# Optimization experiments

Measured on AMD Instinct MI355X. Metric: run time of the kernel, lower is better.

Reference implementation:

```python
import jax, jax.numpy as jnp
import numpy as np

N, M, C, CSKIP, K = 16384, 4096, 256, 128, 3
BIG = 1e10  # distance penalty for cross-batch pairs


def setup_inputs() -> dict:
    key = jax.random.key(0)
    ks = jax.random.split(key, 6)
    return {
        "x": jax.random.normal(ks[0], (M, C), jnp.float32),
        "pos": jax.random.normal(ks[1], (M, 3), jnp.float32),
        "batch": jnp.zeros((M,), jnp.int32),
        "x_skip": jax.random.normal(ks[2], (N, CSKIP), jnp.float32),
        "pos_skip": jax.random.normal(ks[3], (N, 3), jnp.float32),
        "batch_skip": jnp.zeros((N,), jnp.int32),
        "W1": jax.random.normal(ks[4], (C + CSKIP, 256), jnp.float32) * (1.0 / np.sqrt(C + CSKIP)),
        "b1": jnp.zeros((256,), jnp.float32),
        "W2": jax.random.normal(ks[5], (256, 256), jnp.float32) * (1.0 / np.sqrt(256)),
        "b2": jnp.zeros((256,), jnp.float32),
    }


def _knn_idx(pos, pos_skip, batch, batch_skip, k):
    # Squared distances via GEMM form: [N, M]
    a2 = jnp.sum(pos_skip * pos_skip, axis=-1, keepdims=True)      # [N,1]
    b2 = jnp.sum(pos * pos, axis=-1)[None, :]                       # [1,M]
    d2 = a2 + b2 - 2.0 * (pos_skip @ pos.T)                         # [N,M]
    d2 = jnp.where(batch_skip[:, None] != batch[None, :], BIG, d2)
    _, idx = jax.lax.top_k(-d2, k)                                  # [N,k]
    return idx


def reference(x, pos, batch, x_skip, pos_skip, batch_skip, W1, b1, W2, b2):
    idx = _knn_idx(pos, pos_skip, batch, batch_skip, K)             # [N,k] coarse neighbor ids
    # Exact squared dist recomputed from gathered positions (matches torch diff path)
    diff = pos_skip[:, None, :] - pos[idx]                          # [N,k,3]
    d2 = jnp.sum(diff * diff, axis=-1, keepdims=True)               # [N,k,1]
    w = 1.0 / (d2 + 1e-8)                                           # inverse-distance weights
    wsum = jnp.sum(w, axis=1, keepdims=True)                        # per-row scatter_add == sum over k
    w = w / (wsum + 1e-8)
    x_interp = jnp.sum(w * x[idx], axis=1)                          # [N,C]
    h = jnp.concatenate([x_interp, x_skip], axis=1)                 # [N,C+C']
    h = jax.nn.relu(h @ W1 + b1)
    h = jax.nn.relu(h @ W2 + b2)
    return h
```

## Files before the change

### kernel.cpp

```cpp
#include <hip/hip_runtime.h>

typedef float     f4   __attribute__((ext_vector_type(4)));
typedef float     f32x4 __attribute__((ext_vector_type(4)));
typedef _Float16  h8   __attribute__((ext_vector_type(8)));
typedef _Float16  h4   __attribute__((ext_vector_type(4)));
typedef int       i4   __attribute__((ext_vector_type(4)));

#define NQ   16384
#define MP   4096
#define CF   256
#define CSK  128
#define K1   384
#define HID  256
#define QB   16

__global__ __launch_bounds__(256) void knn_kernel(
    const float* __restrict__ pos,
    const float* __restrict__ pos_skip,
    int*   __restrict__ idx_out,
    float* __restrict__ w_out)
{
    __shared__ float          px[MP];
    __shared__ float          py[MP];
    __shared__ float          pz[MP];
    __shared__ unsigned short ci[QB][96];
    __shared__ unsigned short ci2[QB][16][3];

    const int tid = threadIdx.x;

    for (int j = tid; j < MP; j += 256) {
        px[j] = pos[3*j+0];
        py[j] = pos[3*j+1];
        pz[j] = pos[3*j+2];
    }
    __syncthreads();

    const int lane = tid & 63;
    const int wv   = tid >> 6;

    float qx[4], qy[4], qz[4];
    #pragma unroll
    for (int k = 0; k < 4; k++) {
        const int q = blockIdx.x * QB + wv * 4 + k;
        qx[k] = pos_skip[3*q+0];
        qy[k] = pos_skip[3*q+1];
        qz[k] = pos_skip[3*q+2];
    }

    unsigned K0[4], K1v[4], K2[4];
    #pragma unroll
    for (int k = 0; k < 4; k++) { K0[k] = ~0u; K1v[k] = ~0u; K2[k] = ~0u; }

    #define EVAL(PX, PY, PZ, J)                                               \
        _Pragma("unroll")                                                     \
        for (int k = 0; k < 4; k++) {                                         \
            const float dx = qx[k] - (PX), dy = qy[k] - (PY),                 \
                        dz = qz[k] - (PZ);                                    \
            const float dd = fmaf(dx, dx, fmaf(dy, dy, dz * dz));             \
            const unsigned key = (__float_as_uint(dd) & 0xFFFFF000u) | (J);   \
            const unsigned h0 = max(K0[k], key);                              \
            K0[k] = min(K0[k], key);                                          \
            const unsigned n1 = min(K1v[k], h0);                              \
            const unsigned h1 = max(K1v[k], h0);                              \
            K1v[k] = n1;                                                      \
            K2[k] = min(K2[k], h1);                                           \
        }

    float c0x = px[lane],       c1x = px[lane + 64],
          c2x = px[lane + 128], c3x = px[lane + 192];
    float c0y = py[lane],       c1y = py[lane + 64],
          c2y = py[lane + 128], c3y = py[lane + 192];
    float c0z = pz[lane],       c1z = pz[lane + 64],
          c2z = pz[lane + 128], c3z = pz[lane + 192];

    for (int it = 0; it < 64; it += 4) {
        const unsigned jb = it * 64 + lane;
        const float nx0 = px[jb + 256], nx1 = px[jb + 320],
                    nx2 = px[jb + 384], nx3 = px[jb + 448];
        const float ny0 = py[jb + 256], ny1 = py[jb + 320],
                    ny2 = py[jb + 384], ny3 = py[jb + 448];
        const float nz0 = pz[jb + 256], nz1 = pz[jb + 320],
                    nz2 = pz[jb + 384], nz3 = pz[jb + 448];
        EVAL(c0x, c0y, c0z, jb);
        EVAL(c1x, c1y, c1z, jb + 64);
        EVAL(c2x, c2y, c2z, jb + 128);
        EVAL(c3x, c3y, c3z, jb + 192);
        c0x = nx0; c1x = nx1; c2x = nx2; c3x = nx3;
        c0y = ny0; c1y = ny1; c2y = ny2; c3y = ny3;
        c0z = nz0; c1z = nz1; c2z = nz2; c3z = nz3;
    }
    #undef EVAL

    #pragma unroll
    for (int k = 0; k < 4; k++) {
        const unsigned b0 = (unsigned)__builtin_amdgcn_ds_swizzle((int)K0[k],  0x041F);
        const unsigned b1 = (unsigned)__builtin_amdgcn_ds_swizzle((int)K1v[k], 0x041F);
        const unsigned b2 = (unsigned)__builtin_amdgcn_ds_swizzle((int)K2[k],  0x041F);
        const unsigned m0 = min(K0[k], b0);
        const unsigned c1 = max(K0[k], b0);
        const unsigned d0 = min(K1v[k], b1), d1 = max(K1v[k], b1);
        const unsigned m1 = min(c1, d0);
        const unsigned m2 = min(min(max(c1, d0), d1), min(K2[k], b2));
        if (!(lane & 1)) {
            const int q = wv * 4 + k;
            const int pr = lane >> 1;
            ci[q][pr*3+0] = (unsigned short)(m0 & 0xFFFu);
            ci[q][pr*3+1] = (unsigned short)(m1 & 0xFFFu);
            ci[q][pr*3+2] = (unsigned short)(m2 & 0xFFFu);
        }
    }
    __syncthreads();

    {
        const int q    = tid >> 4;
        const int part = tid & 15;
        const int g    = blockIdx.x * QB + q;
        const double qxd = (double)pos_skip[3*g+0];
        const double qyd = (double)pos_skip[3*g+1];
        const double qzd = (double)pos_skip[3*g+2];
        const double a2d = qxd*qxd + qyd*qyd + qzd*qzd;

        double e0 = 1e300, e1 = 1e300, e2 = 1e300;
        int    j0 = 0,     j1 = 0,     j2 = 0;
        #pragma unroll
        for (int c = 0; c < 6; c++) {
            const int j = ci[q][part*6 + c];
            const double pxd = (double)px[j], pyd = (double)py[j],
                         pzd = (double)pz[j];
            const double b2  = pxd*pxd + pyd*pyd + pzd*pzd;
            const double dot = qxd*pxd + qyd*pyd + qzd*pzd;
            const double d   = (a2d + b2) - 2.0 * dot;
            if (d < e2) {
                if (d < e1) {
                    e2 = e1; j2 = j1;
                    if (d < e0) { e1 = e0; j1 = j0; e0 = d; j0 = j; }
                    else        { e1 = d;  j1 = j; }
                } else { e2 = d; j2 = j; }
            }
        }
        ci2[q][part][0] = (unsigned short)j0;
        ci2[q][part][1] = (unsigned short)j1;
        ci2[q][part][2] = (unsigned short)j2;
    }
    __syncthreads();

    if (tid < QB) {
        const int g = blockIdx.x * QB + tid;
        const double qxd = (double)pos_skip[3*g+0];
        const double qyd = (double)pos_skip[3*g+1];
        const double qzd = (double)pos_skip[3*g+2];
        const double a2d = qxd*qxd + qyd*qyd + qzd*qzd;

        double e0 = 1e300, e1 = 1e300, e2 = 1e300;
        int    j0 = 0,     j1 = 0,     j2 = 0;
        for (int p = 0; p < 16; p++) {
            #pragma unroll
            for (int s = 0; s < 3; s++) {
                const int j = ci2[tid][p][s];
                const double pxd = (double)px[j], pyd = (double)py[j],
                             pzd = (double)pz[j];
                const double b2  = pxd*pxd + pyd*pyd + pzd*pzd;
                const double dot = qxd*pxd + qyd*pyd + qzd*pzd;
                const double d   = (a2d + b2) - 2.0 * dot;
                if (d < e2) {
                    if (d < e1) {
                        e2 = e1; j2 = j1;
                        if (d < e0) { e1 = e0; j1 = j0; e0 = d; j0 = j; }
                        else        { e1 = d;  j1 = j; }
                    } else { e2 = d; j2 = j; }
                }
            }
        }
        const float sx = pos_skip[3*g+0], sy = pos_skip[3*g+1], sz = pos_skip[3*g+2];
        const int jj[3] = { j0, j1, j2 };
        float wv3[3];
        #pragma unroll
        for (int k = 0; k < 3; k++) {
            const float dx = sx - px[jj[k]], dy = sy - py[jj[k]],
                        dz = sz - pz[jj[k]];
            const float dd = dx*dx + dy*dy + dz*dz;
            wv3[k] = 1.0f / (dd + 1e-8f);
        }
        const float inv = 1.0f / (wv3[0] + wv3[1] + wv3[2] + 1e-8f);
        #pragma unroll
        for (int k = 0; k < 3; k++) {
            idx_out[g*3+k] = jj[k];
            w_out[g*3+k]   = wv3[k] * inv;
        }
    }
}

__global__ __launch_bounds__(256) void wconv_kernel(
    const float* __restrict__ W1, const float* __restrict__ W2,
    _Float16* __restrict__ Wt1, _Float16* __restrict__ Wt2)
{
    const int i = blockIdx.x * 256 + threadIdx.x;
    if (i < K1 * HID) {
        const int k = i >> 8, n = i & 255;
        Wt1[(size_t)(k >> 5) * 8192 + ((k >> 3) & 3) * 2048 + n * 8 + (k & 7)]
            = (_Float16)W1[i];
    } else {
        const int i2 = i - K1 * HID;
        const int k = i2 >> 8, n = i2 & 255;
        Wt2[(size_t)(k >> 5) * 8192 + ((k >> 3) & 3) * 2048 + n * 8 + (k & 7)]
            = (_Float16)W2[i2];
    }
}

__global__ __launch_bounds__(256) void mlp_kernel(
    const float* __restrict__ x,
    const float* __restrict__ x_skip,
    const _Float16* __restrict__ Wt1,
    const _Float16* __restrict__ Wt2,
    const float* __restrict__ b1,
    const float* __restrict__ b2,
    const int*   __restrict__ nidx,
    const float* __restrict__ nw,
    float* __restrict__ out)
{
    __shared__ _Float16 As[32][392];
    _Float16 (*Hs)[264] = reinterpret_cast<_Float16 (*)[264]>(&As[0][0]);

    const int tid  = threadIdx.x;
    const int row0 = blockIdx.x * 32;

    {
        const int r   = tid >> 3;
        const int sub = tid & 7;
        const int g   = row0 + r;
        const int j0 = nidx[g*3+0], j1 = nidx[g*3+1], j2 = nidx[g*3+2];
        const float w0 = nw[g*3+0], w1 = nw[g*3+1], w2 = nw[g*3+2];
        const f4* xa = (const f4*)(x + (size_t)j0 * CF);
        const f4* xb = (const f4*)(x + (size_t)j1 * CF);
        const f4* xc = (const f4*)(x + (size_t)j2 * CF);
        const f4* xs = (const f4*)(x_skip + (size_t)g * CSK);
        #pragma unroll
        for (int t = 0; t < 8; t++) {
            const int c4 = t * 8 + sub;
            const f4 a = xa[c4], b = xb[c4], c = xc[c4];
            const f4 v = a * w0 + b * w1 + c * w2;
            h4 hv; hv[0]=(_Float16)v[0]; hv[1]=(_Float16)v[1];
                   hv[2]=(_Float16)v[2]; hv[3]=(_Float16)v[3];
            *(h4*)&As[r][c4 * 4] = hv;
        }
        #pragma unroll
        for (int t = 0; t < 4; t++) {
            const int c4 = t * 8 + sub;
            const f4 v = xs[c4];
            h4 hv; hv[0]=(_Float16)v[0]; hv[1]=(_Float16)v[1];
                   hv[2]=(_Float16)v[2]; hv[3]=(_Float16)v[3];
            *(h4*)&As[r][CF + c4 * 4] = hv;
        }
    }

    const int ln   = tid & 15;
    const int quad = (tid >> 4) & 3;
    const int wv_  = tid >> 6;
    const int nb   = wv_ * 64;
    const int q8   = quad * 8;

    const _Float16* w1b = Wt1 + quad * 2048 + (size_t)(nb + ln) * 8;
    const _Float16* w2b = Wt2 + quad * 2048 + (size_t)(nb + ln) * 8;

    f32x4 acc[2][4];
    #pragma unroll
    for (int mt = 0; mt < 2; mt++)
        #pragma unroll
        for (int nt = 0; nt < 4; nt++) acc[mt][nt] = (f32x4)0.0f;

    h8 B[3][4];
    #pragma unroll
    for (int s = 0; s < 3; s++)
        #pragma unroll
        for (int nt = 0; nt < 4; nt++)
            B[s][nt] = *(const h8*)(w1b + (size_t)s * 8192 + nt * 128);

    __syncthreads();

    #pragma unroll
    for (int kb = 0; kb < 12; kb++) {
        const int s = kb % 3;
        h8 ha[2];
        #pragma unroll
        for (int mt = 0; mt < 2; mt++)
            ha[mt] = *(const h8*)&As[mt*16 + ln][kb*32 + q8];
        h8 hb[4];
        #pragma unroll
        for (int nt = 0; nt < 4; nt++) hb[nt] = B[s][nt];
        if (kb < 9) {
            #pragma unroll
            for (int nt = 0; nt < 4; nt++)
                B[s][nt] = *(const h8*)(w1b + (size_t)(kb+3) * 8192 + nt * 128);
        } else {
            #pragma unroll
            for (int nt = 0; nt < 4; nt++)
                B[s][nt] = *(const h8*)(w2b + (size_t)(kb-9) * 8192 + nt * 128);
        }
        #pragma unroll
        for (int mt = 0; mt < 2; mt++)
            #pragma unroll
            for (int nt = 0; nt < 4; nt++)
                acc[mt][nt] = __builtin_amdgcn_mfma_f32_16x16x32_f16(
                    ha[mt], hb[nt], acc[mt][nt], 0, 0, 0);
    }
    __syncthreads();

    #pragma unroll
    for (int nt = 0; nt < 4; nt++) {
        const int n = nb + nt*16 + ln;
        const float bv = b1[n];
        #pragma unroll
        for (int mt = 0; mt < 2; mt++) {
            #pragma unroll
            for (int r = 0; r < 4; r++) {
                const int m = mt*16 + quad*4 + r;
                Hs[m][n] = (_Float16)fmaxf(acc[mt][nt][r] + bv, 0.0f);
            }
            acc[mt][nt] = (f32x4)0.0f;
        }
    }
    __syncthreads();

    #pragma unroll
    for (int kb = 0; kb < 8; kb++) {
        const int s = kb % 3;
        h8 ha[2];
        #pragma unroll
        for (int mt = 0; mt < 2; mt++)
            ha[mt] = *(const h8*)&Hs[mt*16 + ln][kb*32 + q8];
        h8 hb[4];
        #pragma unroll
        for (int nt = 0; nt < 4; nt++) hb[nt] = B[s][nt];
        if (kb < 5) {
            #pragma unroll
            for (int nt = 0; nt < 4; nt++)
                B[s][nt] = *(const h8*)(w2b + (size_t)(kb+3) * 8192 + nt * 128);
        }
        #pragma unroll
        for (int mt = 0; mt < 2; mt++)
            #pragma unroll
            for (int nt = 0; nt < 4; nt++)
                acc[mt][nt] = __builtin_amdgcn_mfma_f32_16x16x32_f16(
                    ha[mt], hb[nt], acc[mt][nt], 0, 0, 0);
    }

    #pragma unroll
    for (int nt = 0; nt < 4; nt++) {
        const int n = nb + nt*16 + ln;
        const float bv = b2[n];
        #pragma unroll
        for (int mt = 0; mt < 2; mt++)
            #pragma unroll
            for (int r = 0; r < 4; r++) {
                const int m = mt*16 + quad*4 + r;
                out[(size_t)(row0 + m) * HID + n] = fmaxf(acc[mt][nt][r] + bv, 0.0f);
            }
    }
}

extern "C" void kernel_launch(void* const* d_in, const int* in_sizes, int n_in,
                              void* d_out, int out_size, void* d_ws, size_t ws_size,
                              hipStream_t stream) {
    const float* x         = (const float*)d_in[0];
    const float* pos       = (const float*)d_in[1];
    const float* x_skip    = (const float*)d_in[3];
    const float* pos_skip  = (const float*)d_in[4];
    const float* W1        = (const float*)d_in[6];
    const float* b1        = (const float*)d_in[7];
    const float* W2        = (const float*)d_in[8];
    const float* b2        = (const float*)d_in[9];
    float* out = (float*)d_out;

    char* ws = (char*)d_ws;
    int*      nidx = (int*)ws;
    float*    nw   = (float*)(ws + 196608);
    _Float16* Wt1  = (_Float16*)(ws + 393216);
    _Float16* Wt2  = (_Float16*)(ws + 589824);

    wconv_kernel<<<(K1*HID + HID*HID) / 256, 256, 0, stream>>>(W1, W2, Wt1, Wt2);
    knn_kernel<<<NQ / QB, 256, 0, stream>>>(pos, pos_skip, nidx, nw);
    mlp_kernel<<<NQ / 32, 256, 0, stream>>>(x, x_skip, Wt1, Wt2, b1, b2, nidx, nw, out);
}
```

Before: 129.7 us.

## Fuse kNN search and MLP into one kernel with 32 queries per block

Merges the kNN kernel and the MLP kernel into a single kernel. Neighbor indices and weights now stay in shared memory instead of going through a global workspace, and the shared memory used for positions is reused for the MLP A/H tiles. Queries per block go from 16 to 32, so each wave tracks 8 queries, which spreads the 48KB position load over more work and halves the kNN grid. The costs are higher register pressure from the 8-query top-3 state, lower occupancy from about 57KB of shared memory, and no overlap between the kNN compute phase and the GEMM phase of other blocks.

```diff
diff --git a/kernel.cpp b/kernel.cpp
--- a/kernel.cpp
+++ b/kernel.cpp
@@ -12,19 +12,45 @@
 #define CSK  128
 #define K1   384
 #define HID  256
-#define QB   16
-
-__global__ __launch_bounds__(256) void knn_kernel(
+
+__global__ __launch_bounds__(256) void wconv_kernel(
+    const float* __restrict__ W1, const float* __restrict__ W2,
+    _Float16* __restrict__ Wt1, _Float16* __restrict__ Wt2)
+{
+    const int i = blockIdx.x * 256 + threadIdx.x;
+    if (i < K1 * HID) {
+        const int k = i >> 8, n = i & 255;
+        Wt1[(size_t)(k >> 5) * 8192 + ((k >> 3) & 3) * 2048 + n * 8 + (k & 7)]
+            = (_Float16)W1[i];
+    } else {
+        const int i2 = i - K1 * HID;
+        const int k = i2 >> 8, n = i2 & 255;
+        Wt2[(size_t)(k >> 5) * 8192 + ((k >> 3) & 3) * 2048 + n * 8 + (k & 7)]
+            = (_Float16)W2[i2];
+    }
+}
+
+__global__ __launch_bounds__(256) void fused_kernel(
     const float* __restrict__ pos,
     const float* __restrict__ pos_skip,
-    int*   __restrict__ idx_out,
-    float* __restrict__ w_out)
+    const float* __restrict__ x,
+    const float* __restrict__ x_skip,
+    const _Float16* __restrict__ Wt1,
+    const _Float16* __restrict__ Wt2,
+    const float* __restrict__ b1,
+    const float* __restrict__ b2,
+    float* __restrict__ out)
 {
-    __shared__ float          px[MP];
-    __shared__ float          py[MP];
-    __shared__ float          pz[MP];
-    __shared__ unsigned short ci[QB][96];
-    __shared__ unsigned short ci2[QB][16][3];
+    __shared__ __align__(16) char smem[57600];
+    float* px = (float*)smem;
+    float* py = (float*)(smem + 16384);
+    float* pz = (float*)(smem + 32768);
+    unsigned short (*ci)[96]    = (unsigned short (*)[96])(smem + 49152);
+    unsigned short (*ci2)[8][3] = (unsigned short (*)[8][3])(smem + 55296);
+    int   (*fidx)[3] = (int (*)[3])(smem + 56832);
+    float (*fw)[3]   = (float (*)[3])(smem + 57216);
+    _Float16 (*As)[392] = (_Float16 (*)[392])smem;
+    _Float16 (*Hs)[264] = (_Float16 (*)[264])smem;
 
     const int tid = threadIdx.x;
 
@@ -38,83 +64,85 @@
     const int lane = tid & 63;
     const int wv   = tid >> 6;
 
-    float qx[4], qy[4], qz[4];
-    #pragma unroll
-    for (int k = 0; k < 4; k++) {
-        const int q = blockIdx.x * QB + wv * 4 + k;
-        qx[k] = pos_skip[3*q+0];
-        qy[k] = pos_skip[3*q+1];
-        qz[k] = pos_skip[3*q+2];
-    }
-
-    unsigned K0[4], K1v[4], K2[4];
-    #pragma unroll
-    for (int k = 0; k < 4; k++) { K0[k] = ~0u; K1v[k] = ~0u; K2[k] = ~0u; }
-
-    #define EVAL(PX, PY, PZ, J)                                               \
-        _Pragma("unroll")                                                     \
-        for (int k = 0; k < 4; k++) {                                         \
-            const float dx = qx[k] - (PX), dy = qy[k] - (PY),                 \
-                        dz = qz[k] - (PZ);                                    \
-            const float dd = fmaf(dx, dx, fmaf(dy, dy, dz * dz));             \
-            const unsigned key = (__float_as_uint(dd) & 0xFFFFF000u) | (J);   \
-            const unsigned h0 = max(K0[k], key);                              \
-            K0[k] = min(K0[k], key);                                          \
-            const unsigned n1 = min(K1v[k], h0);                              \
-            const unsigned h1 = max(K1v[k], h0);                              \
-            K1v[k] = n1;                                                      \
-            K2[k] = min(K2[k], h1);                                           \
-        }
-
-    float c0x = px[lane],       c1x = px[lane + 64],
-          c2x = px[lane + 128], c3x = px[lane + 192];
-    float c0y = py[lane],       c1y = py[lane + 64],
-          c2y = py[lane + 128], c3y = py[lane + 192];
-    float c0z = pz[lane],       c1z = pz[lane + 64],
-          c2z = pz[lane + 128], c3z = pz[lane + 192];
-
-    for (int it = 0; it < 64; it += 4) {
-        const unsigned jb = it * 64 + lane;
-        const float nx0 = px[jb + 256], nx1 = px[jb + 320],
-                    nx2 = px[jb + 384], nx3 = px[jb + 448];
-        const float ny0 = py[jb + 256], ny1 = py[jb + 320],
-                    ny2 = py[jb + 384], ny3 = py[jb + 448];
-        const float nz0 = pz[jb + 256], nz1 = pz[jb + 320],
-                    nz2 = pz[jb + 384], nz3 = pz[jb + 448];
-        EVAL(c0x, c0y, c0z, jb);
-        EVAL(c1x, c1y, c1z, jb + 64);
-        EVAL(c2x, c2y, c2z, jb + 128);
-        EVAL(c3x, c3y, c3z, jb + 192);
-        c0x = nx0; c1x = nx1; c2x = nx2; c3x = nx3;
-        c0y = ny0; c1y = ny1; c2y = ny2; c3y = ny3;
-        c0z = nz0; c1z = nz1; c2z = nz2; c3z = nz3;
-    }
-    #undef EVAL
-
-    #pragma unroll
-    for (int k = 0; k < 4; k++) {
-        const unsigned b0 = (unsigned)__builtin_amdgcn_ds_swizzle((int)K0[k],  0x041F);
-        const unsigned b1 = (unsigned)__builtin_amdgcn_ds_swizzle((int)K1v[k], 0x041F);
-        const unsigned b2 = (unsigned)__builtin_amdgcn_ds_swizzle((int)K2[k],  0x041F);
-        const unsigned m0 = min(K0[k], b0);
-        const unsigned c1 = max(K0[k], b0);
-        const unsigned d0 = min(K1v[k], b1), d1 = max(K1v[k], b1);
-        const unsigned m1 = min(c1, d0);
-        const unsigned m2 = min(min(max(c1, d0), d1), min(K2[k], b2));
-        if (!(lane & 1)) {
-            const int q = wv * 4 + k;
-            const int pr = lane >> 1;
-            ci[q][pr*3+0] = (unsigned short)(m0 & 0xFFFu);
-            ci[q][pr*3+1] = (unsigned short)(m1 & 0xFFFu);
-            ci[q][pr*3+2] = (unsigned short)(m2 & 0xFFFu);
-        }
-    }
-    __syncthreads();
-
     {
-        const int q    = tid >> 4;
-        const int part = tid & 15;
-        const int g    = blockIdx.x * QB + q;
+        float qx[8], qy[8], qz[8];
+        #pragma unroll
+        for (int k = 0; k < 8; k++) {
+            const int q = blockIdx.x * 32 + wv * 8 + k;
+            qx[k] = pos_skip[3*q+0];
+            qy[k] = pos_skip[3*q+1];
+            qz[k] = pos_skip[3*q+2];
+        }
+
+        unsigned K0[8], K1v[8], K2[8];
+        #pragma unroll
+        for (int k = 0; k < 8; k++) { K0[k] = ~0u; K1v[k] = ~0u; K2[k] = ~0u; }
+
+        #define EVAL(PX, PY, PZ, J)                                           \
+            _Pragma("unroll")                                                 \
+            for (int k = 0; k < 8; k++) {                                     \
+                const float dx = qx[k] - (PX), dy = qy[k] - (PY),             \
+                            dz = qz[k] - (PZ);                                \
+                const float dd = fmaf(dx, dx, fmaf(dy, dy, dz * dz));         \
+                const unsigned key = (__float_as_uint(dd) & 0xFFFFF000u) | (J);\
+                const unsigned h0 = max(K0[k], key);                          \
+                K0[k] = min(K0[k], key);                                      \
+                const unsigned n1 = min(K1v[k], h0);                          \
+                const unsigned h1 = max(K1v[k], h0);                          \
+                K1v[k] = n1;                                                  \
+                K2[k] = min(K2[k], h1);                                       \
+            }
+
+        float c0x = px[lane],       c1x = px[lane + 64],
+              c2x = px[lane + 128], c3x = px[lane + 192];
+        float c0y = py[lane],       c1y = py[lane + 64],
+              c2y = py[lane + 128], c3y = py[lane + 192];
+        float c0z = pz[lane],       c1z = pz[lane + 64],
+              c2z = pz[lane + 128], c3z = pz[lane + 192];
+
+        for (int it = 0; it < 64; it += 4) {
+            const unsigned jb = it * 64 + lane;
+            const float nx0 = px[jb + 256], nx1 = px[jb + 320],
+                        nx2 = px[jb + 384], nx3 = px[jb + 448];
+            const float ny0 = py[jb + 256], ny1 = py[jb + 320],
+                        ny2 = py[jb + 384], ny3 = py[jb + 448];
+            const float nz0 = pz[jb + 256], nz1 = pz[jb + 320],
+                        nz2 = pz[jb + 384], nz3 = pz[jb + 448];
+            EVAL(c0x, c0y, c0z, jb);
+            EVAL(c1x, c1y, c1z, jb + 64);
+            EVAL(c2x, c2y, c2z, jb + 128);
+            EVAL(c3x, c3y, c3z, jb + 192);
+            c0x = nx0; c1x = nx1; c2x = nx2; c3x = nx3;
+            c0y = ny0; c1y = ny1; c2y = ny2; c3y = ny3;
+            c0z = nz0; c1z = nz1; c2z = nz2; c3z = nz3;
+        }
+        #undef EVAL
+
+        #pragma unroll
+        for (int k = 0; k < 8; k++) {
+            const unsigned b0 = (unsigned)__builtin_amdgcn_ds_swizzle((int)K0[k],  0x041F);
+            const unsigned b1 = (unsigned)__builtin_amdgcn_ds_swizzle((int)K1v[k], 0x041F);
+            const unsigned b2 = (unsigned)__builtin_amdgcn_ds_swizzle((int)K2[k],  0x041F);
+            const unsigned m0 = min(K0[k], b0);
+            const unsigned c1 = max(K0[k], b0);
+            const unsigned d0 = min(K1v[k], b1), d1 = max(K1v[k], b1);
+            const unsigned m1 = min(c1, d0);
+            const unsigned m2 = min(min(max(c1, d0), d1), min(K2[k], b2));
+            if (!(lane & 1)) {
+                const int q = wv * 8 + k;
+                const int pr = lane >> 1;
+                ci[q][pr*3+0] = (unsigned short)(m0 & 0xFFFu);
+                ci[q][pr*3+1] = (unsigned short)(m1 & 0xFFFu);
+                ci[q][pr*3+2] = (unsigned short)(m2 & 0xFFFu);
+            }
+        }
+    }
+    __syncthreads();
+
+    {
+        const int q    = tid >> 3;
+        const int part = tid & 7;
+        const int g    = blockIdx.x * 32 + q;
         const double qxd = (double)pos_skip[3*g+0];
         const double qyd = (double)pos_skip[3*g+1];
         const double qzd = (double)pos_skip[3*g+2];
@@ -123,8 +151,8 @@
         double e0 = 1e300, e1 = 1e300, e2 = 1e300;
         int    j0 = 0,     j1 = 0,     j2 = 0;
         #pragma unroll
-        for (int c = 0; c < 6; c++) {
-            const int j = ci[q][part*6 + c];
+        for (int c = 0; c < 12; c++) {
+            const int j = ci[q][part*12 + c];
             const double pxd = (double)px[j], pyd = (double)py[j],
                          pzd = (double)pz[j];
             const double b2  = pxd*pxd + pyd*pyd + pzd*pzd;
@@ -144,8 +172,8 @@
     }
     __syncthreads();
 
-    if (tid < QB) {
-        const int g = blockIdx.x * QB + tid;
+    if (tid < 32) {
+        const int g = blockIdx.x * 32 + tid;
         const double qxd = (double)pos_skip[3*g+0];
         const double qyd = (double)pos_skip[3*g+1];
         const double qzd = (double)pos_skip[3*g+2];
@@ -153,7 +181,7 @@
 
         double e0 = 1e300, e1 = 1e300, e2 = 1e300;
         int    j0 = 0,     j1 = 0,     j2 = 0;
-        for (int p = 0; p < 16; p++) {
+        for (int p = 0; p < 8; p++) {
             #pragma unroll
             for (int s = 0; s < 3; s++) {
                 const int j = ci2[tid][p][s];
@@ -184,56 +212,23 @@
         const float inv = 1.0f / (wv3[0] + wv3[1] + wv3[2] + 1e-8f);
         #pragma unroll
         for (int k = 0; k < 3; k++) {
-            idx_out[g*3+k] = jj[k];
-            w_out[g*3+k]   = wv3[k] * inv;
-        }
-    }
-}
-
-__global__ __launch_bounds__(256) void wconv_kernel(
-    const float* __restrict__ W1, const float* __restrict__ W2,
-    _Float16* __restrict__ Wt1, _Float16* __restrict__ Wt2)
-{
-    const int i = blockIdx.x * 256 + threadIdx.x;
-    if (i < K1 * HID) {
-        const int k = i >> 8, n = i & 255;
-        Wt1[(size_t)(k >> 5) * 8192 + ((k >> 3) & 3) * 2048 + n * 8 + (k & 7)]
-            = (_Float16)W1[i];
-    } else {
-        const int i2 = i - K1 * HID;
-        const int k = i2 >> 8, n = i2 & 255;
-        Wt2[(size_t)(k >> 5) * 8192 + ((k >> 3) & 3) * 2048 + n * 8 + (k & 7)]
-            = (_Float16)W2[i2];
-    }
-}
-
-__global__ __launch_bounds__(256) void mlp_kernel(
-    const float* __restrict__ x,
-    const float* __restrict__ x_skip,
-    const _Float16* __restrict__ Wt1,
-    const _Float16* __restrict__ Wt2,
-    const float* __restrict__ b1,
-    const float* __restrict__ b2,
-    const int*   __restrict__ nidx,
-    const float* __restrict__ nw,
-    float* __restrict__ out)
-{
-    __shared__ _Float16 As[32][392];
-    _Float16 (*Hs)[264] = reinterpret_cast<_Float16 (*)[264]>(&As[0][0]);
-
-    const int tid  = threadIdx.x;
+            fidx[tid][k] = jj[k];
+            fw[tid][k]   = wv3[k] * inv;
+        }
+    }
+    __syncthreads();
+
     const int row0 = blockIdx.x * 32;
 
     {
         const int r   = tid >> 3;
         const int sub = tid & 7;
-        const int g   = row0 + r;
-        const int j0 = nidx[g*3+0], j1 = nidx[g*3+1], j2 = nidx[g*3+2];
-        const float w0 = nw[g*3+0], w1 = nw[g*3+1], w2 = nw[g*3+2];
+        const int j0 = fidx[r][0], j1 = fidx[r][1], j2 = fidx[r][2];
+        const float w0 = fw[r][0], w1 = fw[r][1], w2 = fw[r][2];
         const f4* xa = (const f4*)(x + (size_t)j0 * CF);
         const f4* xb = (const f4*)(x + (size_t)j1 * CF);
         const f4* xc = (const f4*)(x + (size_t)j2 * CF);
-        const f4* xs = (const f4*)(x_skip + (size_t)g * CSK);
+        const f4* xs = (const f4*)(x_skip + (size_t)(row0 + r) * CSK);
         #pragma unroll
         for (int t = 0; t < 8; t++) {
             const int c4 = t * 8 + sub;
@@ -255,8 +250,7 @@
 
     const int ln   = tid & 15;
     const int quad = (tid >> 4) & 3;
-    const int wv_  = tid >> 6;
-    const int nb   = wv_ * 64;
+    const int nb   = wv * 64;
     const int q8   = quad * 8;
 
     const _Float16* w1b = Wt1 + quad * 2048 + (size_t)(nb + ln) * 8;
@@ -372,12 +366,10 @@
     float* out = (float*)d_out;
 
     char* ws = (char*)d_ws;
-    int*      nidx = (int*)ws;
-    float*    nw   = (float*)(ws + 196608);
-    _Float16* Wt1  = (_Float16*)(ws + 393216);
-    _Float16* Wt2  = (_Float16*)(ws + 589824);
+    _Float16* Wt1 = (_Float16*)ws;
+    _Float16* Wt2 = (_Float16*)(ws + 196608);
 
     wconv_kernel<<<(K1*HID + HID*HID) / 256, 256, 0, stream>>>(W1, W2, Wt1, Wt2);
-    knn_kernel<<<NQ / QB, 256, 0, stream>>>(pos, pos_skip, nidx, nw);
-    mlp_kernel<<<NQ / 32, 256, 0, stream>>>(x, x_skip, Wt1, Wt2, b1, b2, nidx, nw, out);
+    fused_kernel<<<NQ / 32, 256, 0, stream>>>(pos, pos_skip, x, x_skip,
+                                              Wt1, Wt2, b1, b2, out);
 }
```

Result: faster. 122.5 us (-5.5%).
